# Kernel optimization log

Hardware: AMD Instinct MI355X
Metric: run time of the kernel (lower is better)

## Reference

```python
import jax, jax.numpy as jnp
import numpy as np

N = 20000      # nodes
E = 320000     # edges
H = 512        # hidden_dim = input_dim
G = 400        # graphs in batch
NMAX = 50      # n_max_nodes
NCOND = 8
L = 3          # n_layers
BN_EPS = 1e-5


def setup_inputs() -> dict:
    key = jax.random.key(0)
    ks = jax.random.split(key, 20)
    x = jax.random.normal(ks[0], (N, H), dtype=jnp.float32)
    edge_index = jax.random.randint(ks[1], (2, E), 0, N, dtype=jnp.int32)
    batch = jnp.sort(jax.random.randint(ks[2], (N,), 0, G, dtype=jnp.int32))
    stats = jax.random.normal(ks[3], (G, NCOND), dtype=jnp.float32)
    adj = jax.random.normal(ks[4], (G, NMAX, NMAX), dtype=jnp.float32)
    s = 0.02
    w1 = jax.random.normal(ks[5], (L, H, H), dtype=jnp.float32) * s
    b1 = jnp.zeros((L, H), dtype=jnp.float32)
    a1 = jnp.full((L,), 0.25, dtype=jnp.float32)          # PReLU scalar slope
    bn_gamma = jnp.ones((L, H), dtype=jnp.float32)
    bn_beta = jnp.zeros((L, H), dtype=jnp.float32)
    bn_mean = jax.random.normal(ks[6], (L, H), dtype=jnp.float32) * 0.1
    bn_var = jax.random.uniform(ks[7], (L, H), dtype=jnp.float32) + 0.5
    w2 = jax.random.normal(ks[8], (L, H, H), dtype=jnp.float32) * s
    b2 = jnp.zeros((L, H), dtype=jnp.float32)
    a2 = jnp.full((L,), 0.25, dtype=jnp.float32)
    fin = H + NCOND + NMAX * NMAX
    fc1_w = jax.random.normal(ks[9], (fin, H // 2), dtype=jnp.float32) * s
    fc1_b = jnp.zeros((H // 2,), dtype=jnp.float32)
    fc2_w = jax.random.normal(ks[10], (H // 2, 1), dtype=jnp.float32) * s
    fc2_b = jnp.zeros((1,), dtype=jnp.float32)
    return dict(x=x, edge_index=edge_index, batch=batch, stats=stats, adj=adj,
                w1=w1, b1=b1, a1=a1, bn_gamma=bn_gamma, bn_beta=bn_beta,
                bn_mean=bn_mean, bn_var=bn_var, w2=w2, b2=b2, a2=a2,
                fc1_w=fc1_w, fc1_b=fc1_b, fc2_w=fc2_w, fc2_b=fc2_b)


def _prelu(x, a):
    return jnp.where(x >= 0, x, a * x)


def reference(x, edge_index, batch, stats, adj,
              w1, b1, a1, bn_gamma, bn_beta, bn_mean, bn_var,
              w2, b2, a2, fc1_w, fc1_b, fc2_w, fc2_b):
    src, dst = edge_index[0], edge_index[1]
    h = x
    for l in range(L):
        # GINConv (eps=0): (1+eps)*x + sum of neighbor messages
        agg = jax.ops.segment_sum(h[src], dst, num_segments=N)
        h = h + agg
        # MLP: Linear -> PReLU -> BatchNorm1d (eval, running stats) -> Linear -> PReLU
        h = _prelu(h @ w1[l] + b1[l], a1[l])
        h = (h - bn_mean[l]) * (bn_gamma[l] / jnp.sqrt(bn_var[l] + BN_EPS)) + bn_beta[l]
        h = _prelu(h @ w2[l] + b2[l], a2[l])
        h = jax.nn.relu(h)  # dropout is identity in eval mode
    pooled = jax.ops.segment_sum(h, batch, num_segments=G)      # global_add_pool
    x_cat = jnp.concatenate([pooled, stats, adj.reshape(G, -1)], axis=1)
    x_l = jax.nn.relu(x_cat @ fc1_w + fc1_b)
    out = jax.nn.sigmoid(x_l @ fc2_w + fc2_b)
    return (out, x_l)
```

## Files before the change

### kernel.cpp

```cpp
#include <hip/hip_runtime.h>
#include <cstdint>
#include <cstddef>

#define NN 20000
#define NE 320000
#define HD 512
#define NG 400
#define NHID ((size_t)NN * HD)
#define FCK 3072
#define FCN 256

typedef __attribute__((ext_vector_type(4))) float f32x4;
typedef __attribute__((ext_vector_type(2))) float f32x2;
typedef __attribute__((ext_vector_type(8))) short s16x8;
typedef __attribute__((ext_vector_type(4))) short s16x4;
typedef __attribute__((ext_vector_type(2))) unsigned int u32x2;

#if defined(__has_builtin)
#if __has_builtin(__builtin_amdgcn_cvt_pk_f32_fp8)
#define HAS_HW_FP8 1
#endif
#endif

__device__ __forceinline__ unsigned short f2bf(float f) {
  uint32_t u = __builtin_bit_cast(uint32_t, f);
  uint32_t r = u + 0x7fffu + ((u >> 16) & 1u);
  return (unsigned short)(r >> 16);
}
__device__ __forceinline__ float bf2f(unsigned short h) {
  return __builtin_bit_cast(float, (uint32_t)h << 16);
}

__device__ __forceinline__ uint32_t f32_to_fp8(float f) {
  float af = fabsf(f);
  af = fminf(af, 440.f);
  uint32_t u = __builtin_bit_cast(uint32_t, af);
  u += 0x7ffffu + ((u >> 20) & 1u);
  uint32_t e = u >> 23;
  uint32_t out = (e < 121u) ? 0u : (((e - 120u) << 3) | ((u >> 20) & 7u));
  return out | ((__builtin_bit_cast(uint32_t, f) >> 24) & 0x80u);
}
__device__ __forceinline__ float fp8_to_f32_sw(uint32_t b) {
  uint32_t e = (b >> 3) & 0xfu;
  uint32_t u = ((b & 0x80u) << 24) | ((e + 120u) << 23) | ((b & 7u) << 20);
  return e ? __builtin_bit_cast(float, u) : 0.f;
}
__device__ __forceinline__ void dec8(u32x2 v, float* f) {
#ifdef HAS_HW_FP8
  f32x2 p0 = __builtin_amdgcn_cvt_pk_f32_fp8(v[0], false);
  f32x2 p1 = __builtin_amdgcn_cvt_pk_f32_fp8(v[0], true);
  f32x2 p2 = __builtin_amdgcn_cvt_pk_f32_fp8(v[1], false);
  f32x2 p3 = __builtin_amdgcn_cvt_pk_f32_fp8(v[1], true);
  f[0] = p0[0]; f[1] = p0[1]; f[2] = p1[0]; f[3] = p1[1];
  f[4] = p2[0]; f[5] = p2[1]; f[6] = p3[0]; f[7] = p3[1];
#else
  #pragma unroll
  for (int k = 0; k < 4; ++k) f[k] = fp8_to_f32_sw((v[0] >> (8 * k)) & 0xffu);
  #pragma unroll
  for (int k = 0; k < 4; ++k) f[4 + k] = fp8_to_f32_sw((v[1] >> (8 * k)) & 0xffu);
#endif
}

__global__ void cast_x_kernel(const float* __restrict__ in, unsigned char* __restrict__ outp) {
  size_t i = ((size_t)blockIdx.x * 256 + threadIdx.x) * 4;
  f32x4 v = *(const f32x4*)(in + i);
  uint32_t o = 0;
  #pragma unroll
  for (int j = 0; j < 4; ++j) o |= f32_to_fp8(v[j]) << (8 * j);
  *(uint32_t*)(outp + i) = o;
}

__global__ __launch_bounds__(256) void transpose_w12_kernel(
    const float* __restrict__ w1, const float* __restrict__ w2,
    unsigned short* __restrict__ w1t, unsigned short* __restrict__ w2t) {
  __shared__ float tl[64][65];
  int z = blockIdx.z;
  const float* ip = (z < 3 ? w1 + (size_t)z * 262144 : w2 + (size_t)(z - 3) * 262144);
  unsigned short* op = (z < 3 ? w1t + (size_t)z * 262144 : w2t + (size_t)(z - 3) * 262144);
  int k0 = blockIdx.x * 64;
  int j0 = blockIdx.y * 64;
  int t = threadIdx.x;
  int c = t & 63, r4 = t >> 6;
  #pragma unroll
  for (int rr = 0; rr < 16; ++rr) {
    int r = rr * 4 + r4;
    tl[r][c] = ip[(size_t)(k0 + r) * 512 + j0 + c];
  }
  __syncthreads();
  #pragma unroll
  for (int jj = 0; jj < 16; ++jj) {
    int j = jj * 4 + r4;
    op[(size_t)(j0 + j) * 512 + k0 + c] = f2bf(tl[c][j]);
  }
}

__global__ __launch_bounds__(256) void transpose_fc1_kernel(
    const float* __restrict__ in, unsigned short* __restrict__ outp) {
  __shared__ float tl[64][65];
  int k0 = blockIdx.x * 64;
  int j0 = blockIdx.y * 64;
  int t = threadIdx.x;
  int c = t & 63, r4 = t >> 6;
  #pragma unroll
  for (int rr = 0; rr < 16; ++rr) {
    int r = rr * 4 + r4;
    int k = k0 + r;
    tl[r][c] = (k < 3020) ? in[(size_t)k * FCN + j0 + c] : 0.f;
  }
  __syncthreads();
  #pragma unroll
  for (int jj = 0; jj < 16; ++jj) {
    int j = jj * 4 + r4;
    outp[(size_t)(j0 + j) * FCK + k0 + c] = f2bf(tl[c][j]);
  }
}

__global__ void hist_kernel(const int* __restrict__ ei, int* __restrict__ deg) {
  int e = blockIdx.x * 256 + threadIdx.x;
  if (e >= NE) return;
  atomicAdd(&deg[ei[NE + e]], 1);
}

__global__ __launch_bounds__(1024) void scan_kernel(const int* __restrict__ deg,
                                                    int* __restrict__ rowptr,
                                                    int* __restrict__ cursor) {
  __shared__ int s[1024];
  int t = threadIdx.x;
  int base = t * 20;
  int local[20];
  int sum = 0;
  #pragma unroll
  for (int i = 0; i < 20; ++i) {
    int idx = base + i;
    int d = idx < NN ? deg[idx] : 0;
    local[i] = sum;
    sum += d;
  }
  s[t] = sum;
  __syncthreads();
  for (int off = 1; off < 1024; off <<= 1) {
    int v = (t >= off) ? s[t - off] : 0;
    __syncthreads();
    s[t] += v;
    __syncthreads();
  }
  int pre = (t > 0) ? s[t - 1] : 0;
  #pragma unroll
  for (int i = 0; i < 20; ++i) {
    int idx = base + i;
    if (idx < NN) {
      rowptr[idx] = pre + local[i];
      cursor[idx] = pre + local[i];
    }
  }
  if (t == 1023) rowptr[NN] = s[1023];
}

__global__ void fill_kernel(const int* __restrict__ ei, int* __restrict__ cursor,
                            int* __restrict__ col) {
  int e = blockIdx.x * 256 + threadIdx.x;
  if (e >= NE) return;
  int src = ei[e];
  int dst = ei[NE + e];
  int p = atomicAdd(&cursor[dst], 1);
  col[p] = src;
}

__global__ __launch_bounds__(256) void gather_kernel(
    const unsigned char* __restrict__ h8, const int* __restrict__ rowptr,
    const int* __restrict__ col, unsigned short* __restrict__ hs) {
  int n = blockIdx.x * 4 + (threadIdx.x >> 6);
  int lane = threadIdx.x & 63;
  if (n >= NN) return;
  int lo = rowptr[n], hi = rowptr[n + 1];
  const unsigned char* hl = h8 + (size_t)(lane << 3);
  u32x2 sv = *(const u32x2*)(hl + (size_t)n * 512);
  float a0[8], a1[8], tmp[8];
  dec8(sv, a0);
  #pragma unroll
  for (int i = 0; i < 8; ++i) a1[i] = 0.f;
  int j = lo;
  for (; j + 4 <= hi; j += 4) {
    int c0 = col[j], c1 = col[j + 1], c2 = col[j + 2], c3 = col[j + 3];
    u32x2 v0 = *(const u32x2*)(hl + (size_t)c0 * 512);
    u32x2 v1 = *(const u32x2*)(hl + (size_t)c1 * 512);
    u32x2 v2 = *(const u32x2*)(hl + (size_t)c2 * 512);
    u32x2 v3 = *(const u32x2*)(hl + (size_t)c3 * 512);
    dec8(v0, tmp);
    #pragma unroll
    for (int i = 0; i < 8; ++i) a0[i] += tmp[i];
    dec8(v1, tmp);
    #pragma unroll
    for (int i = 0; i < 8; ++i) a1[i] += tmp[i];
    dec8(v2, tmp);
    #pragma unroll
    for (int i = 0; i < 8; ++i) a0[i] += tmp[i];
    dec8(v3, tmp);
    #pragma unroll
    for (int i = 0; i < 8; ++i) a1[i] += tmp[i];
  }
  for (; j < hi; ++j) {
    u32x2 v0 = *(const u32x2*)(hl + (size_t)col[j] * 512);
    dec8(v0, tmp);
    #pragma unroll
    for (int i = 0; i < 8; ++i) a0[i] += tmp[i];
  }
  s16x8 o;
  #pragma unroll
  for (int i = 0; i < 8; ++i) o[i] = (short)f2bf(a0[i] + a1[i]);
  *(s16x8*)(hs + (size_t)n * HD + (lane << 3)) = o;
}

template <int EPI>
__global__ __launch_bounds__(256, 2) void gemm_bf16(
    const unsigned short* __restrict__ A, const unsigned short* __restrict__ Bt,
    const float* __restrict__ bias, const float* __restrict__ slope,
    const float* __restrict__ bnm, const float* __restrict__ bnv,
    const float* __restrict__ bng, const float* __restrict__ bnb,
    void* __restrict__ Cout, int M) {
  __shared__ unsigned short lds[16384];
  char* ldsb = (char*)lds;
  const int tid = threadIdx.x;
  const int lane = tid & 63;
  const int wid = tid >> 6;
  const int wm = wid >> 1, wn = wid & 1;

  const unsigned bid = blockIdx.x;
  const unsigned nwg = gridDim.x;
  const unsigned q = nwg >> 3, r = nwg & 7;
  const unsigned xcd = bid & 7, idx = bid >> 3;
  const unsigned wgid = (xcd < r ? xcd * (q + 1) : r * (q + 1) + (xcd - r) * q) + idx;
  const int m0 = (int)(wgid >> 2) * 128;
  const int n0 = (int)(wgid & 3) * 128;

  f32x4 acc[4][4];
  #pragma unroll
  for (int m = 0; m < 4; ++m)
    #pragma unroll
    for (int n = 0; n < 4; ++n) acc[m][n] = (f32x4){0.f, 0.f, 0.f, 0.f};

  const int row_s = tid >> 3;
  const int slot_s = tid & 7;
  const unsigned ldso_w = (unsigned)(wid << 10);

  for (int kk = 0; kk < HD; kk += 64) {
    __syncthreads();
    #pragma unroll
    for (int i = 0; i < 4; ++i) {
      int ra = i * 32 + row_s;
      int rga = m0 + ra; rga = rga < M ? rga : M - 1;
      const unsigned short* ga = A + (size_t)rga * HD + (kk + ((slot_s ^ (ra & 7)) << 3));
      __builtin_amdgcn_global_load_lds(
          (const __attribute__((address_space(1))) unsigned int*)(const void*)ga,
          (__attribute__((address_space(3))) unsigned int*)(void*)(ldsb + (unsigned)(i * 4096) + ldso_w),
          16, 0, 0);
    }
    #pragma unroll
    for (int i = 0; i < 4; ++i) {
      int rb = i * 32 + row_s;
      const unsigned short* gb = Bt + (size_t)(n0 + rb) * HD + (kk + ((slot_s ^ (rb & 7)) << 3));
      __builtin_amdgcn_global_load_lds(
          (const __attribute__((address_space(1))) unsigned int*)(const void*)gb,
          (__attribute__((address_space(3))) unsigned int*)(void*)(ldsb + 16384u + (unsigned)(i * 4096) + ldso_w),
          16, 0, 0);
    }
    __syncthreads();

    const unsigned swz = (unsigned)((lane & 7) << 4);
    const unsigned koff = (unsigned)((lane >> 4) << 4);
    const unsigned arow = (unsigned)((wm * 64 + (lane & 15)) * 128);
    const unsigned brow = 16384u + (unsigned)((wn * 64 + (lane & 15)) * 128);
    #pragma unroll
    for (int s = 0; s < 2; ++s) {
      s16x8 af[4], bfr[4];
      #pragma unroll
      for (int m = 0; m < 4; ++m)
        af[m] = *(const s16x8*)(ldsb + ((arow + (unsigned)(m * 2048 + s * 64) + koff) ^ swz));
      #pragma unroll
      for (int n = 0; n < 4; ++n)
        bfr[n] = *(const s16x8*)(ldsb + ((brow + (unsigned)(n * 2048 + s * 64) + koff) ^ swz));
      #pragma unroll
      for (int m = 0; m < 4; ++m)
        #pragma unroll
        for (int n = 0; n < 4; ++n)
          acc[m][n] = __builtin_amdgcn_mfma_f32_16x16x32_bf16(af[m], bfr[n], acc[m][n], 0, 0, 0);
    }
  }

  const float al = slope[0];
  const int colb = n0 + wn * 64 + (lane & 15);
  const int rowb = m0 + wm * 64 + ((lane >> 4) << 2);
  #pragma unroll
  for (int n = 0; n < 4; ++n) {
    const int j = colb + n * 16;
    const float bi = bias[j];
    float sc = 1.f, sh = 0.f;
    if (EPI == 1) {
      sc = bng[j] * (1.f / sqrtf(bnv[j] + 1e-5f));
      sh = bnb[j] - bnm[j] * sc;
    }
    #pragma unroll
    for (int m = 0; m < 4; ++m) {
      #pragma unroll
      for (int r2 = 0; r2 < 4; ++r2) {
        int row = rowb + m * 16 + r2;
        if (row < M) {
          float v = acc[m][n][r2] + bi;
          v = v >= 0.f ? v : al * v;
          if (EPI == 1) v = v * sc + sh;
          else v = fmaxf(v, 0.f);
          if (EPI == 4)
            ((unsigned char*)Cout)[(size_t)row * HD + j] = (unsigned char)f32_to_fp8(v);
          else
            ((unsigned short*)Cout)[(size_t)row * HD + j] = f2bf(v);
        }
      }
    }
  }
}

__global__ __launch_bounds__(256, 2) void fc_gemm_kernel(
    const unsigned short* __restrict__ A, const unsigned short* __restrict__ Bt,
    float* __restrict__ part) {
  __shared__ unsigned short lds[16384];
  char* ldsb = (char*)lds;
  const int tid = threadIdx.x;
  const int lane = tid & 63;
  const int wid = tid >> 6;
  const int wm = wid >> 1, wn = wid & 1;
  const int m0 = blockIdx.x * 128;
  const int n0 = blockIdx.y * 128;
  const int kbase = blockIdx.z * 512;

  f32x4 acc[4][4];
  #pragma unroll
  for (int m = 0; m < 4; ++m)
    #pragma unroll
    for (int n = 0; n < 4; ++n) acc[m][n] = (f32x4){0.f, 0.f, 0.f, 0.f};

  const int row_s = tid >> 3;
  const int slot_s = tid & 7;
  const unsigned ldso_w = (unsigned)(wid << 10);

  for (int kk = kbase; kk < kbase + 512; kk += 64) {
    __syncthreads();
    #pragma unroll
    for (int i = 0; i < 4; ++i) {
      int ra = i * 32 + row_s;
      int rga = m0 + ra; rga = rga < NG ? rga : NG - 1;
      const unsigned short* ga = A + (size_t)rga * FCK + (kk + ((slot_s ^ (ra & 7)) << 3));
      __builtin_amdgcn_global_load_lds(
          (const __attribute__((address_space(1))) unsigned int*)(const void*)ga,
          (__attribute__((address_space(3))) unsigned int*)(void*)(ldsb + (unsigned)(i * 4096) + ldso_w),
          16, 0, 0);
    }
    #pragma unroll
    for (int i = 0; i < 4; ++i) {
      int rb = i * 32 + row_s;
      const unsigned short* gb = Bt + (size_t)(n0 + rb) * FCK + (kk + ((slot_s ^ (rb & 7)) << 3));
      __builtin_amdgcn_global_load_lds(
          (const __attribute__((address_space(1))) unsigned int*)(const void*)gb,
          (__attribute__((address_space(3))) unsigned int*)(void*)(ldsb + 16384u + (unsigned)(i * 4096) + ldso_w),
          16, 0, 0);
    }
    __syncthreads();

    const unsigned swz = (unsigned)((lane & 7) << 4);
    const unsigned koff = (unsigned)((lane >> 4) << 4);
    const unsigned arow = (unsigned)((wm * 64 + (lane & 15)) * 128);
    const unsigned brow = 16384u + (unsigned)((wn * 64 + (lane & 15)) * 128);
    #pragma unroll
    for (int s = 0; s < 2; ++s) {
      s16x8 af[4], bfr[4];
      #pragma unroll
      for (int m = 0; m < 4; ++m)
        af[m] = *(const s16x8*)(ldsb + ((arow + (unsigned)(m * 2048 + s * 64) + koff) ^ swz));
      #pragma unroll
      for (int n = 0; n < 4; ++n)
        bfr[n] = *(const s16x8*)(ldsb + ((brow + (unsigned)(n * 2048 + s * 64) + koff) ^ swz));
      #pragma unroll
      for (int m = 0; m < 4; ++m)
        #pragma unroll
        for (int n = 0; n < 4; ++n)
          acc[m][n] = __builtin_amdgcn_mfma_f32_16x16x32_bf16(af[m], bfr[n], acc[m][n], 0, 0, 0);
    }
  }

  float* po = part + (size_t)blockIdx.z * (NG * FCN);
  const int colb = n0 + wn * 64 + (lane & 15);
  const int rowb = m0 + wm * 64 + ((lane >> 4) << 2);
  #pragma unroll
  for (int n = 0; n < 4; ++n) {
    const int j = colb + n * 16;
    #pragma unroll
    for (int m = 0; m < 4; ++m) {
      #pragma unroll
      for (int r = 0; r < 4; ++r) {
        int row = rowb + m * 16 + r;
        if (row < NG) po[(size_t)row * FCN + j] = acc[m][n][r];
      }
    }
  }
}

__device__ __forceinline__ int lbound(const int* __restrict__ a, int n, int v) {
  int lo = 0, hi = n;
  while (lo < hi) { int m = (lo + hi) >> 1; if (a[m] < v) lo = m + 1; else hi = m; }
  return lo;
}

__global__ __launch_bounds__(256) void pool_xcat_kernel(
    const unsigned short* __restrict__ hs, const int* __restrict__ batch,
    const float* __restrict__ stats, const float* __restrict__ adj,
    unsigned short* __restrict__ xcat) {
  int g = blockIdx.x, t = threadIdx.x;
  int lo = lbound(batch, NN, g);
  int hi = lbound(batch, NN, g + 1);
  float s0 = 0.f, s1 = 0.f;
  for (int n = lo; n < hi; ++n) {
    uint32_t v = *(const uint32_t*)(hs + (size_t)n * HD + 2 * t);
    s0 += bf2f((unsigned short)(v & 0xffffu));
    s1 += bf2f((unsigned short)(v >> 16));
  }
  unsigned short* row = xcat + (size_t)g * FCK;
  row[2 * t] = f2bf(s0);
  row[2 * t + 1] = f2bf(s1);
  if (t < 8) row[HD + t] = f2bf(stats[g * 8 + t]);
  for (int i = t; i < 2500; i += 256) row[520 + i] = f2bf(adj[(size_t)g * 2500 + i]);
  if (t < 52) row[3020 + t] = 0;
}

__global__ __launch_bounds__(256) void fc_epi_kernel(
    const float* __restrict__ part, const float* __restrict__ b1,
    const float* __restrict__ w2, const float* __restrict__ b2,
    float* __restrict__ outp) {
  __shared__ float red[256];
  int g = blockIdx.x, t = threadIdx.x;
  float s = b1[t];
  #pragma unroll
  for (int ks = 0; ks < 6; ++ks) s += part[(size_t)ks * (NG * FCN) + g * FCN + t];
  float xl = fmaxf(s, 0.f);
  outp[NG + g * FCN + t] = xl;
  red[t] = xl * w2[t];
  __syncthreads();
  for (int st = 128; st > 0; st >>= 1) {
    if (t < st) red[t] += red[t + st];
    __syncthreads();
  }
  if (t == 0) outp[g] = 1.f / (1.f + expf(-(red[0] + b2[0])));
}

extern "C" void kernel_launch(void* const* d_in, const int* in_sizes, int n_in,
                              void* d_out, int out_size, void* d_ws, size_t ws_size,
                              hipStream_t stream) {
  const float* x = (const float*)d_in[0];
  const int* ei = (const int*)d_in[1];
  const int* batch = (const int*)d_in[2];
  const float* stats = (const float*)d_in[3];
  const float* adj = (const float*)d_in[4];
  const float* w1 = (const float*)d_in[5];
  const float* b1 = (const float*)d_in[6];
  const float* a1 = (const float*)d_in[7];
  const float* bng = (const float*)d_in[8];
  const float* bnb = (const float*)d_in[9];
  const float* bnm = (const float*)d_in[10];
  const float* bnv = (const float*)d_in[11];
  const float* w2 = (const float*)d_in[12];
  const float* b2 = (const float*)d_in[13];
  const float* a2 = (const float*)d_in[14];
  const float* fc1w = (const float*)d_in[15];
  const float* fc1b = (const float*)d_in[16];
  const float* fc2w = (const float*)d_in[17];
  const float* fc2b = (const float*)d_in[18];
  float* outp = (float*)d_out;

  char* ws = (char*)d_ws;
  unsigned char* h8 = (unsigned char*)ws;     ws += NHID;
  unsigned short* hsb = (unsigned short*)ws;  ws += NHID * 2;
  unsigned short* h1b = (unsigned short*)ws;  ws += NHID * 2;
  unsigned short* w1t = (unsigned short*)ws;  ws += (size_t)3 * 512 * 512 * 2;
  unsigned short* w2t = (unsigned short*)ws;  ws += (size_t)3 * 512 * 512 * 2;
  int* deg = (int*)ws;                        ws += (size_t)NN * 4;
  int* rowptr = (int*)ws;                     ws += (size_t)(NN + 4) * 4;
  int* cursor = (int*)ws;                     ws += (size_t)NN * 4;
  int* col = (int*)ws;                        ws += (size_t)NE * 4;
  unsigned short* xcat = (unsigned short*)ws; ws += (size_t)NG * FCK * 2;
  unsigned short* fc1t = (unsigned short*)ws; ws += (size_t)FCN * FCK * 2;
  float* fcpart = (float*)ws;                 ws += (size_t)6 * NG * FCN * 4;

  hipMemsetAsync(deg, 0, (size_t)NN * 4, stream);
  hist_kernel<<<(NE + 255) / 256, 256, 0, stream>>>(ei, deg);
  scan_kernel<<<1, 1024, 0, stream>>>(deg, rowptr, cursor);
  fill_kernel<<<(NE + 255) / 256, 256, 0, stream>>>(ei, cursor, col);

  cast_x_kernel<<<(int)(NHID / 1024), 256, 0, stream>>>(x, h8);
  transpose_w12_kernel<<<dim3(8, 8, 6), 256, 0, stream>>>(w1, w2, w1t, w2t);
  transpose_fc1_kernel<<<dim3(FCK / 64, FCN / 64, 1), 256, 0, stream>>>(fc1w, fc1t);

  for (int l = 0; l < 3; ++l) {
    gather_kernel<<<NN / 4, 256, 0, stream>>>(h8, rowptr, col, hsb);
    gemm_bf16<1><<<628, 256, 0, stream>>>(hsb, w1t + (size_t)l * 262144,
        b1 + l * 512, a1 + l, bnm + l * 512, bnv + l * 512, bng + l * 512, bnb + l * 512,
        (void*)h1b, NN);
    if (l < 2) {
      gemm_bf16<4><<<628, 256, 0, stream>>>(h1b, w2t + (size_t)l * 262144,
          b2 + l * 512, a2 + l, nullptr, nullptr, nullptr, nullptr, (void*)h8, NN);
    } else {
      gemm_bf16<2><<<628, 256, 0, stream>>>(h1b, w2t + (size_t)l * 262144,
          b2 + l * 512, a2 + l, nullptr, nullptr, nullptr, nullptr, (void*)hsb, NN);
    }
  }

  pool_xcat_kernel<<<NG, 256, 0, stream>>>(hsb, batch, stats, adj, xcat);
  fc_gemm_kernel<<<dim3(4, 2, 6), 256, 0, stream>>>(xcat, fc1t, fcpart);
  fc_epi_kernel<<<NG, 256, 0, stream>>>(fcpart, fc1b, fc2w, fc2b, outp);
}
```

Before: 347.4 us.

## Double-buffer LDS tiles in bf16 GEMM to overlap loads with MFMA

Grows the GEMM shared-memory buffer to hold two K-tiles. The loop now prefetches the next 64-wide K slice with global_load_lds into the alternate buffer while MFMAs run on the current one, using one barrier per iteration instead of two. The aim is to hide global-to-LDS latency behind compute. In exchange, LDS use per block doubles to 64 KB, which can limit occupancy at two blocks per CU. Correctness also relies on the end-of-iteration barrier waiting for the async LDS loads to finish.

```diff
diff --git a/kernel.cpp b/kernel.cpp
--- a/kernel.cpp
+++ b/kernel.cpp
@@ -211,6 +211,31 @@
   *(s16x8*)(hs + (size_t)n * HD + (lane << 3)) = o;
 }
 
+#define STAGE_TILE(kkv, bufbase)                                                          \
+  do {                                                                                    \
+    int kk_ = (kkv);                                                                      \
+    unsigned bb_ = (bufbase);                                                             \
+    _Pragma("unroll")                                                                     \
+    for (int i = 0; i < 4; ++i) {                                                         \
+      int ra = i * 32 + row_s;                                                            \
+      int rga = m0 + ra; rga = rga < M ? rga : M - 1;                                     \
+      const unsigned short* ga = A + (size_t)rga * HD + (kk_ + ((slot_s ^ (ra & 7)) << 3)); \
+      __builtin_amdgcn_global_load_lds(                                                   \
+          (const __attribute__((address_space(1))) unsigned int*)(const void*)ga,         \
+          (__attribute__((address_space(3))) unsigned int*)(void*)(ldsb + bb_ + (unsigned)(i * 4096) + ldso_w), \
+          16, 0, 0);                                                                      \
+    }                                                                                     \
+    _Pragma("unroll")                                                                     \
+    for (int i = 0; i < 4; ++i) {                                                         \
+      int rb = i * 32 + row_s;                                                            \
+      const unsigned short* gb = Bt + (size_t)(n0 + rb) * HD + (kk_ + ((slot_s ^ (rb & 7)) << 3)); \
+      __builtin_amdgcn_global_load_lds(                                                   \
+          (const __attribute__((address_space(1))) unsigned int*)(const void*)gb,         \
+          (__attribute__((address_space(3))) unsigned int*)(void*)(ldsb + bb_ + 16384u + (unsigned)(i * 4096) + ldso_w), \
+          16, 0, 0);                                                                      \
+    }                                                                                     \
+  } while (0)
+
 template <int EPI>
 __global__ __launch_bounds__(256, 2) void gemm_bf16(
     const unsigned short* __restrict__ A, const unsigned short* __restrict__ Bt,
@@ -218,7 +243,7 @@
     const float* __restrict__ bnm, const float* __restrict__ bnv,
     const float* __restrict__ bng, const float* __restrict__ bnb,
     void* __restrict__ Cout, int M) {
-  __shared__ unsigned short lds[16384];
+  __shared__ unsigned short lds[32768];
   char* ldsb = (char*)lds;
   const int tid = threadIdx.x;
   const int lane = tid & 63;
@@ -243,48 +268,35 @@
   const int slot_s = tid & 7;
   const unsigned ldso_w = (unsigned)(wid << 10);
 
-  for (int kk = 0; kk < HD; kk += 64) {
-    __syncthreads();
-    #pragma unroll
-    for (int i = 0; i < 4; ++i) {
-      int ra = i * 32 + row_s;
-      int rga = m0 + ra; rga = rga < M ? rga : M - 1;
-      const unsigned short* ga = A + (size_t)rga * HD + (kk + ((slot_s ^ (ra & 7)) << 3));
-      __builtin_amdgcn_global_load_lds(
-          (const __attribute__((address_space(1))) unsigned int*)(const void*)ga,
-          (__attribute__((address_space(3))) unsigned int*)(void*)(ldsb + (unsigned)(i * 4096) + ldso_w),
-          16, 0, 0);
-    }
-    #pragma unroll
-    for (int i = 0; i < 4; ++i) {
-      int rb = i * 32 + row_s;
-      const unsigned short* gb = Bt + (size_t)(n0 + rb) * HD + (kk + ((slot_s ^ (rb & 7)) << 3));
-      __builtin_amdgcn_global_load_lds(
-          (const __attribute__((address_space(1))) unsigned int*)(const void*)gb,
-          (__attribute__((address_space(3))) unsigned int*)(void*)(ldsb + 16384u + (unsigned)(i * 4096) + ldso_w),
-          16, 0, 0);
-    }
-    __syncthreads();
-
-    const unsigned swz = (unsigned)((lane & 7) << 4);
-    const unsigned koff = (unsigned)((lane >> 4) << 4);
-    const unsigned arow = (unsigned)((wm * 64 + (lane & 15)) * 128);
-    const unsigned brow = 16384u + (unsigned)((wn * 64 + (lane & 15)) * 128);
+  const unsigned swz = (unsigned)((lane & 7) << 4);
+  const unsigned koff = (unsigned)((lane >> 4) << 4);
+  const unsigned arow = (unsigned)((wm * 64 + (lane & 15)) * 128);
+  const unsigned brow = 16384u + (unsigned)((wn * 64 + (lane & 15)) * 128);
+
+  STAGE_TILE(0, 0u);
+  __syncthreads();
+
+  unsigned cur = 0;
+  for (int kt = 0; kt < 8; ++kt) {
+    if (kt < 7) STAGE_TILE((kt + 1) * 64, (cur ^ 1u) * 32768u);
+    const unsigned base = cur * 32768u;
     #pragma unroll
     for (int s = 0; s < 2; ++s) {
       s16x8 af[4], bfr[4];
       #pragma unroll
       for (int m = 0; m < 4; ++m)
-        af[m] = *(const s16x8*)(ldsb + ((arow + (unsigned)(m * 2048 + s * 64) + koff) ^ swz));
+        af[m] = *(const s16x8*)(ldsb + base + ((arow + (unsigned)(m * 2048 + s * 64) + koff) ^ swz));
       #pragma unroll
       for (int n = 0; n < 4; ++n)
-        bfr[n] = *(const s16x8*)(ldsb + ((brow + (unsigned)(n * 2048 + s * 64) + koff) ^ swz));
+        bfr[n] = *(const s16x8*)(ldsb + base + ((brow + (unsigned)(n * 2048 + s * 64) + koff) ^ swz));
       #pragma unroll
       for (int m = 0; m < 4; ++m)
         #pragma unroll
         for (int n = 0; n < 4; ++n)
           acc[m][n] = __builtin_amdgcn_mfma_f32_16x16x32_bf16(af[m], bfr[n], acc[m][n], 0, 0, 0);
     }
+    __syncthreads();
+    cur ^= 1u;
   }
 
   const float al = slope[0];
```

After: 402.5 us. 1.16x slower.
